# Optimization experiments

Measured on AMD Instinct MI355X. Metric: run time of the kernel, lower is better.

The kernel has to match this reference:

```python
import jax, jax.numpy as jnp
import numpy as np

B = 16          # number of sequences
L = 2048        # tokens per sequence (uniform here; math handles ragged)
D = 4096        # hidden size (GritLM-7B)
TOTAL = B * L   # flattened total tokens
EPS = 1e-12     # torch F.normalize eps (PoolerHead normalize=True)


def setup_inputs() -> dict:
    key = jax.random.key(0)
    k1, k2 = jax.random.split(key)
    hidden_states = jax.random.normal(k1, (TOTAL, D), dtype=jnp.float32)
    prompt_lens = jnp.full((B,), L, dtype=jnp.int32)          # sum == TOTAL
    instruction_lens = jax.random.randint(k2, (B,), 1, 33, dtype=jnp.int32)
    return {
        "hidden_states": hidden_states,
        "prompt_lens": prompt_lens,
        "instruction_lens": instruction_lens,
    }


def reference(hidden_states, prompt_lens, instruction_lens):
    # hidden_states: [total_tokens, D]; prompt_lens/instruction_lens: [B]
    n = hidden_states.shape[0]
    ends = jnp.cumsum(prompt_lens)          # [B] exclusive segment ends
    starts = ends - prompt_lens             # [B] segment starts
    pos = jnp.arange(n)
    seg = jnp.searchsorted(ends, pos, side="right")  # [total] segment id per token
    pos_in_seg = pos - starts[seg]
    # mask out the first instruction_len tokens of each sequence
    mask = pos_in_seg >= instruction_lens[seg]
    masked = jnp.where(mask[:, None], hidden_states, jnp.zeros((), hidden_states.dtype))
    sums = jax.ops.segment_sum(masked, seg, num_segments=prompt_lens.shape[0])  # [B, D]
    counts = (prompt_lens - instruction_lens).astype(hidden_states.dtype)        # [B]
    mean = sums / counts[:, None]
    # PoolerHead(normalize=True): L2 normalize per sequence
    norm = jnp.maximum(jnp.linalg.norm(mean, axis=-1, keepdims=True), EPS)
    return mean / norm
```

## Files before the change

kernel.cpp:

```cpp
#include <hip/hip_runtime.h>
#include <math.h>

#define TPB 256
#define ROW_CHUNKS 32

__global__ void __launch_bounds__(TPB) grit_partial_kernel(
    const float* __restrict__ hs,
    const int* __restrict__ plens,
    const int* __restrict__ ilens,
    float* __restrict__ partials,
    int B, int D)
{
    const int b  = blockIdx.z;
    const int ry = blockIdx.y;
    const int plen = plens[b];
    const int ilen = ilens[b];

    int start = 0;
    for (int i = 0; i < b; ++i) start += plens[i];

    const int rpc = (plen + ROW_CHUNKS - 1) / ROW_CHUNKS;
    int r_lo = ry * rpc;
    int r_hi = r_lo + rpc;
    if (r_hi > plen) r_hi = plen;
    if (r_lo < ilen) r_lo = ilen;

    const int col = (blockIdx.x * TPB + threadIdx.x) * 4;
    if (col >= D) return;

    float4 a0 = make_float4(0.f, 0.f, 0.f, 0.f);
    float4 a1 = a0, a2 = a0, a3 = a0;

    if (r_lo < r_hi) {
        const size_t stride = (size_t)D * sizeof(float);
        const char* p = (const char*)(hs + (size_t)(start + r_lo) * (size_t)D + col);
        int r = r_lo;
        for (; r + 4 <= r_hi; r += 4) {
            const float4 v0 = *(const float4*)(p);
            const float4 v1 = *(const float4*)(p + stride);
            const float4 v2 = *(const float4*)(p + 2 * stride);
            const float4 v3 = *(const float4*)(p + 3 * stride);
            p += 4 * stride;
            a0.x += v0.x; a0.y += v0.y; a0.z += v0.z; a0.w += v0.w;
            a1.x += v1.x; a1.y += v1.y; a1.z += v1.z; a1.w += v1.w;
            a2.x += v2.x; a2.y += v2.y; a2.z += v2.z; a2.w += v2.w;
            a3.x += v3.x; a3.y += v3.y; a3.z += v3.z; a3.w += v3.w;
        }
        for (; r < r_hi; ++r) {
            const float4 v = *(const float4*)(p);
            p += stride;
            a0.x += v.x; a0.y += v.y; a0.z += v.z; a0.w += v.w;
        }
    }

    float4 t;
    t.x = (a0.x + a1.x) + (a2.x + a3.x);
    t.y = (a0.y + a1.y) + (a2.y + a3.y);
    t.z = (a0.z + a1.z) + (a2.z + a3.z);
    t.w = (a0.w + a1.w) + (a2.w + a3.w);

    *(float4*)(partials + (size_t)(b * ROW_CHUNKS + ry) * (size_t)D + col) = t;
}

__global__ void __launch_bounds__(TPB) grit_finalize_kernel(
    const int* __restrict__ plens,
    const int* __restrict__ ilens,
    const float* __restrict__ partials,
    float* __restrict__ out,
    int D)
{
    const int b = blockIdx.x;
    const float inv = 1.0f / (float)(plens[b] - ilens[b]);

    const float* __restrict__ p = partials + (size_t)b * ROW_CHUNKS * (size_t)D;
    float* __restrict__ o = out + (size_t)b * (size_t)D;

    float sq = 0.f;
    for (int col = threadIdx.x * 4; col < D; col += TPB * 4) {
        float4 s = make_float4(0.f, 0.f, 0.f, 0.f);
        #pragma unroll
        for (int ry = 0; ry < ROW_CHUNKS; ++ry) {
            const float4 v = *(const float4*)(p + (size_t)ry * (size_t)D + col);
            s.x += v.x; s.y += v.y; s.z += v.z; s.w += v.w;
        }
        float4 m;
        m.x = s.x * inv; m.y = s.y * inv; m.z = s.z * inv; m.w = s.w * inv;
        sq += m.x * m.x + m.y * m.y + m.z * m.z + m.w * m.w;
        *(float4*)(o + col) = m;
    }

    #pragma unroll
    for (int off = 32; off > 0; off >>= 1)
        sq += __shfl_down(sq, off, 64);

    __shared__ float wsum[TPB / 64];
    const int lane = threadIdx.x & 63;
    const int wave = threadIdx.x >> 6;
    if (lane == 0) wsum[wave] = sq;
    __syncthreads();

    float total = 0.f;
    #pragma unroll
    for (int w = 0; w < TPB / 64; ++w) total += wsum[w];

    const float invn = 1.0f / fmaxf(sqrtf(total), 1e-12f);

    for (int col = threadIdx.x * 4; col < D; col += TPB * 4) {
        const float4 m = *(const float4*)(o + col);
        float4 r;
        r.x = m.x * invn; r.y = m.y * invn; r.z = m.z * invn; r.w = m.w * invn;
        *(float4*)(o + col) = r;
    }
}

extern "C" void kernel_launch(void* const* d_in, const int* in_sizes, int n_in,
                              void* d_out, int out_size, void* d_ws, size_t ws_size,
                              hipStream_t stream) {
    const float* hs    = (const float*)d_in[0];
    const int*   plens = (const int*)d_in[1];
    const int*   ilens = (const int*)d_in[2];
    float*       out   = (float*)d_out;

    const int B = in_sizes[1];
    const int D = out_size / B;

    float* partials = (float*)d_ws;

    const int col_chunks = (D + TPB * 4 - 1) / (TPB * 4);
    dim3 grid(col_chunks, ROW_CHUNKS, B);
    grit_partial_kernel<<<grid, TPB, 0, stream>>>(hs, plens, ilens, partials, B, D);

    grit_finalize_kernel<<<B, TPB, 0, stream>>>(plens, ilens, partials, out, D);
}
```

Measured before the change: 676.8 us.

## Specialize partial sum for D=4096 with full-row blocks and split finalize

Adds a D=4096 partial kernel in which each block covers a full row: every thread loads 4 float4 per row and handles two rows per iteration, giving 8 loads in flight. Row chunks per sequence rise from 32 to 64 to keep the same total block count with wider blocks. The single-block-per-sequence finalize is split into a column-parallel reduce kernel that writes per-block squared-norm partials, plus a small normalize kernel. The cost is an extra launch and twice as many partials to write and read back.

```diff
diff --git a/kernel.cpp b/kernel.cpp
--- a/kernel.cpp
+++ b/kernel.cpp
@@ -2,91 +2,132 @@
 #include <math.h>
 
 #define TPB 256
-#define ROW_CHUNKS 32
+#define RC 64
 
-__global__ void __launch_bounds__(TPB) grit_partial_kernel(
+__global__ void __launch_bounds__(TPB) grit_partial4096(
     const float* __restrict__ hs,
     const int* __restrict__ plens,
     const int* __restrict__ ilens,
-    float* __restrict__ partials,
-    int B, int D)
+    float* __restrict__ partials)
 {
-    const int b  = blockIdx.z;
-    const int ry = blockIdx.y;
+    const int D = 4096;
+    const int b  = blockIdx.y;
+    const int ry = blockIdx.x;
     const int plen = plens[b];
     const int ilen = ilens[b];
 
     int start = 0;
     for (int i = 0; i < b; ++i) start += plens[i];
 
-    const int rpc = (plen + ROW_CHUNKS - 1) / ROW_CHUNKS;
+    const int rpc = (plen + RC - 1) / RC;
     int r_lo = ry * rpc;
     int r_hi = r_lo + rpc;
     if (r_hi > plen) r_hi = plen;
     if (r_lo < ilen) r_lo = ilen;
 
+    const int t = threadIdx.x;
+    float4 A0 = make_float4(0.f,0.f,0.f,0.f), A1 = A0, A2 = A0, A3 = A0;
+    float4 B0 = A0, B1 = A0, B2 = A0, B3 = A0;
+
+    if (r_lo < r_hi) {
+        const float* rp = hs + (size_t)(start + r_lo) * (size_t)D + t * 4;
+        int r = r_lo;
+        for (; r + 2 <= r_hi; r += 2) {
+            const float4 v0 = *(const float4*)(rp);
+            const float4 v1 = *(const float4*)(rp + 1024);
+            const float4 v2 = *(const float4*)(rp + 2048);
+            const float4 v3 = *(const float4*)(rp + 3072);
+            const float4 w0 = *(const float4*)(rp + 4096);
+            const float4 w1 = *(const float4*)(rp + 4096 + 1024);
+            const float4 w2 = *(const float4*)(rp + 4096 + 2048);
+            const float4 w3 = *(const float4*)(rp + 4096 + 3072);
+            rp += 8192;
+            A0.x += v0.x; A0.y += v0.y; A0.z += v0.z; A0.w += v0.w;
+            A1.x += v1.x; A1.y += v1.y; A1.z += v1.z; A1.w += v1.w;
+            A2.x += v2.x; A2.y += v2.y; A2.z += v2.z; A2.w += v2.w;
+            A3.x += v3.x; A3.y += v3.y; A3.z += v3.z; A3.w += v3.w;
+            B0.x += w0.x; B0.y += w0.y; B0.z += w0.z; B0.w += w0.w;
+            B1.x += w1.x; B1.y += w1.y; B1.z += w1.z; B1.w += w1.w;
+            B2.x += w2.x; B2.y += w2.y; B2.z += w2.z; B2.w += w2.w;
+            B3.x += w3.x; B3.y += w3.y; B3.z += w3.z; B3.w += w3.w;
+        }
+        if (r < r_hi) {
+            const float4 v0 = *(const float4*)(rp);
+            const float4 v1 = *(const float4*)(rp + 1024);
+            const float4 v2 = *(const float4*)(rp + 2048);
+            const float4 v3 = *(const float4*)(rp + 3072);
+            A0.x += v0.x; A0.y += v0.y; A0.z += v0.z; A0.w += v0.w;
+            A1.x += v1.x; A1.y += v1.y; A1.z += v1.z; A1.w += v1.w;
+            A2.x += v2.x; A2.y += v2.y; A2.z += v2.z; A2.w += v2.w;
+            A3.x += v3.x; A3.y += v3.y; A3.z += v3.z; A3.w += v3.w;
+        }
+    }
+    A0.x += B0.x; A0.y += B0.y; A0.z += B0.z; A0.w += B0.w;
+    A1.x += B1.x; A1.y += B1.y; A1.z += B1.z; A1.w += B1.w;
+    A2.x += B2.x; A2.y += B2.y; A2.z += B2.z; A2.w += B2.w;
+    A3.x += B3.x; A3.y += B3.y; A3.z += B3.z; A3.w += B3.w;
+
+    float* dst = partials + (size_t)(b * RC + ry) * (size_t)D + t * 4;
+    *(float4*)(dst)        = A0;
+    *(float4*)(dst + 1024) = A1;
+    *(float4*)(dst + 2048) = A2;
+    *(float4*)(dst + 3072) = A3;
+}
+
+__global__ void __launch_bounds__(TPB) grit_partial_generic(
+    const float* __restrict__ hs,
+    const int* __restrict__ plens,
+    const int* __restrict__ ilens,
+    float* __restrict__ partials,
+    int D)
+{
+    const int b  = blockIdx.z;
+    const int ry = blockIdx.y;
+    const int plen = plens[b];
+    const int ilen = ilens[b];
+    int start = 0;
+    for (int i = 0; i < b; ++i) start += plens[i];
+    const int rpc = (plen + RC - 1) / RC;
+    int r_lo = ry * rpc;
+    int r_hi = r_lo + rpc;
+    if (r_hi > plen) r_hi = plen;
+    if (r_lo < ilen) r_lo = ilen;
     const int col = (blockIdx.x * TPB + threadIdx.x) * 4;
     if (col >= D) return;
-
-    float4 a0 = make_float4(0.f, 0.f, 0.f, 0.f);
-    float4 a1 = a0, a2 = a0, a3 = a0;
-
-    if (r_lo < r_hi) {
-        const size_t stride = (size_t)D * sizeof(float);
-        const char* p = (const char*)(hs + (size_t)(start + r_lo) * (size_t)D + col);
-        int r = r_lo;
-        for (; r + 4 <= r_hi; r += 4) {
-            const float4 v0 = *(const float4*)(p);
-            const float4 v1 = *(const float4*)(p + stride);
-            const float4 v2 = *(const float4*)(p + 2 * stride);
-            const float4 v3 = *(const float4*)(p + 3 * stride);
-            p += 4 * stride;
-            a0.x += v0.x; a0.y += v0.y; a0.z += v0.z; a0.w += v0.w;
-            a1.x += v1.x; a1.y += v1.y; a1.z += v1.z; a1.w += v1.w;
-            a2.x += v2.x; a2.y += v2.y; a2.z += v2.z; a2.w += v2.w;
-            a3.x += v3.x; a3.y += v3.y; a3.z += v3.z; a3.w += v3.w;
-        }
-        for (; r < r_hi; ++r) {
-            const float4 v = *(const float4*)(p);
-            p += stride;
-            a0.x += v.x; a0.y += v.y; a0.z += v.z; a0.w += v.w;
-        }
+    float4 a = make_float4(0.f,0.f,0.f,0.f);
+    for (int r = r_lo; r < r_hi; ++r) {
+        const float4 v = *(const float4*)(hs + (size_t)(start + r) * (size_t)D + col);
+        a.x += v.x; a.y += v.y; a.z += v.z; a.w += v.w;
     }
-
-    float4 t;
-    t.x = (a0.x + a1.x) + (a2.x + a3.x);
-    t.y = (a0.y + a1.y) + (a2.y + a3.y);
-    t.z = (a0.z + a1.z) + (a2.z + a3.z);
-    t.w = (a0.w + a1.w) + (a2.w + a3.w);
-
-    *(float4*)(partials + (size_t)(b * ROW_CHUNKS + ry) * (size_t)D + col) = t;
+    *(float4*)(partials + (size_t)(b * RC + ry) * (size_t)D + col) = a;
 }
 
-__global__ void __launch_bounds__(TPB) grit_finalize_kernel(
+__global__ void __launch_bounds__(TPB) grit_reduce_kernel(
     const int* __restrict__ plens,
     const int* __restrict__ ilens,
     const float* __restrict__ partials,
     float* __restrict__ out,
-    int D)
+    float* __restrict__ sqws,
+    int D, int CX)
 {
-    const int b = blockIdx.x;
+    const int b  = blockIdx.y;
+    const int cx = blockIdx.x;
+    const int c  = cx * (TPB * 4) + threadIdx.x * 4;
     const float inv = 1.0f / (float)(plens[b] - ilens[b]);
 
-    const float* __restrict__ p = partials + (size_t)b * ROW_CHUNKS * (size_t)D;
-    float* __restrict__ o = out + (size_t)b * (size_t)D;
-
     float sq = 0.f;
-    for (int col = threadIdx.x * 4; col < D; col += TPB * 4) {
-        float4 s = make_float4(0.f, 0.f, 0.f, 0.f);
-        #pragma unroll
-        for (int ry = 0; ry < ROW_CHUNKS; ++ry) {
-            const float4 v = *(const float4*)(p + (size_t)ry * (size_t)D + col);
+    if (c < D) {
+        const float* p = partials + (size_t)b * RC * (size_t)D + c;
+        float4 s = make_float4(0.f,0.f,0.f,0.f);
+        #pragma unroll 8
+        for (int ry = 0; ry < RC; ++ry) {
+            const float4 v = *(const float4*)(p + (size_t)ry * (size_t)D);
             s.x += v.x; s.y += v.y; s.z += v.z; s.w += v.w;
         }
         float4 m;
         m.x = s.x * inv; m.y = s.y * inv; m.z = s.z * inv; m.w = s.w * inv;
-        sq += m.x * m.x + m.y * m.y + m.z * m.z + m.w * m.w;
-        *(float4*)(o + col) = m;
+        sq = m.x*m.x + m.y*m.y + m.z*m.z + m.w*m.w;
+        *(float4*)(out + (size_t)b * (size_t)D + c) = m;
     }
 
     #pragma unroll
@@ -99,17 +140,29 @@
     if (lane == 0) wsum[wave] = sq;
     __syncthreads();
 
+    if (threadIdx.x == 0) {
+        float total = 0.f;
+        #pragma unroll
+        for (int w = 0; w < TPB / 64; ++w) total += wsum[w];
+        sqws[b * CX + cx] = total;
+    }
+}
+
+__global__ void __launch_bounds__(TPB) grit_norm_kernel(
+    const float* __restrict__ sqws,
+    float* __restrict__ out,
+    int D, int CX)
+{
+    const int b = blockIdx.x;
     float total = 0.f;
-    #pragma unroll
-    for (int w = 0; w < TPB / 64; ++w) total += wsum[w];
-
+    for (int i = 0; i < CX; ++i) total += sqws[b * CX + i];
     const float invn = 1.0f / fmaxf(sqrtf(total), 1e-12f);
 
+    float* o = out + (size_t)b * (size_t)D;
     for (int col = threadIdx.x * 4; col < D; col += TPB * 4) {
-        const float4 m = *(const float4*)(o + col);
-        float4 r;
-        r.x = m.x * invn; r.y = m.y * invn; r.z = m.z * invn; r.w = m.w * invn;
-        *(float4*)(o + col) = r;
+        float4 m = *(const float4*)(o + col);
+        m.x *= invn; m.y *= invn; m.z *= invn; m.w *= invn;
+        *(float4*)(o + col) = m;
     }
 }
 
@@ -125,10 +178,19 @@
     const int D = out_size / B;
 
     float* partials = (float*)d_ws;
+    float* sqws     = partials + (size_t)B * RC * (size_t)D;
+    const int CX = (D + TPB * 4 - 1) / (TPB * 4);
 
-    const int col_chunks = (D + TPB * 4 - 1) / (TPB * 4);
-    dim3 grid(col_chunks, ROW_CHUNKS, B);
-    grit_partial_kernel<<<grid, TPB, 0, stream>>>(hs, plens, ilens, partials, B, D);
+    if (D == 4096) {
+        dim3 grid(RC, B);
+        grit_partial4096<<<grid, TPB, 0, stream>>>(hs, plens, ilens, partials);
+    } else {
+        dim3 grid(CX, RC, B);
+        grit_partial_generic<<<grid, TPB, 0, stream>>>(hs, plens, ilens, partials, D);
+    }
 
-    grit_finalize_kernel<<<B, TPB, 0, stream>>>(plens, ilens, partials, out, D);
+    dim3 rgrid(CX, B);
+    grit_reduce_kernel<<<rgrid, TPB, 0, stream>>>(plens, ilens, partials, out, sqws, D, CX);
+
+    grit_norm_kernel<<<B, TPB, 0, stream>>>(sqws, out, D, CX);
 }
```

New measurement: 683.0 us. Within noise of the previous version (+0.9%).
